# Optimization experiments

Measured on AMD Instinct MI355X. Metric: run time of the kernel, lower is better.

Reference implementation:

```python
import jax, jax.numpy as jnp
import numpy as np
import math

B, N, D, H = 256, 2048, 128, 8
HD = D // H  # 16
TANH_CLIP = 10.0
TEMP = 1.0


def setup_inputs() -> dict:
    key = jax.random.key(0)
    ks = jax.random.split(key, 10)
    context_node_projected = jax.random.normal(ks[0], (B, 1, D), dtype=jnp.float32)
    node_embeddings = jax.random.normal(ks[1], (B, N, D), dtype=jnp.float32)
    glimpse_K = jax.random.normal(ks[2], (H, B, 1, N, HD), dtype=jnp.float32)
    glimpse_V = jax.random.normal(ks[3], (H, B, 1, N, HD), dtype=jnp.float32)
    logit_K = jax.random.normal(ks[4], (B, 1, N, D), dtype=jnp.float32)
    W_ctx = jax.random.normal(ks[5], (2 * D, D), dtype=jnp.float32) * 0.05
    W_out = jax.random.normal(ks[6], (D, D), dtype=jnp.float32) * 0.05
    first_a = jax.random.randint(ks[7], (B, 1), 0, N, dtype=jnp.int32)
    current_node = jax.random.randint(ks[8], (B, 1), 0, N, dtype=jnp.int32)
    mask = jax.random.uniform(ks[9], (B, 1, N)) < 0.3
    mask = mask.at[:, :, 0].set(False)  # guarantee at least one feasible node
    return {
        "context_node_projected": context_node_projected,
        "node_embeddings": node_embeddings,
        "glimpse_K": glimpse_K,
        "glimpse_V": glimpse_V,
        "logit_K": logit_K,
        "W_ctx": W_ctx,
        "W_out": W_out,
        "first_a": first_a,
        "current_node": current_node,
        "mask": mask,
    }


def reference(context_node_projected, node_embeddings, glimpse_K, glimpse_V,
              logit_K, W_ctx, W_out, first_a, current_node, mask):
    # --- step context: gather first and current node embeddings (i > 0 branch) ---
    idx = jnp.concatenate([first_a, current_node], axis=1)          # [B, 2]
    ctx = jnp.take_along_axis(node_embeddings, idx[:, :, None], axis=1)  # [B, 2, D]
    ctx = ctx.reshape(ctx.shape[0], 1, 2 * ctx.shape[-1])           # [B, 1, 2D]
    query = context_node_projected + ctx @ W_ctx                    # [B, 1, D]

    b, steps, d = query.shape
    # glimpse_Q: [H, B, steps, 1, HD]
    glimpse_Q = query.reshape(b, steps, H, 1, HD).transpose(2, 0, 1, 3, 4)
    # compatibility: [H, B, steps, 1, N]
    compat = jnp.matmul(glimpse_Q, jnp.swapaxes(glimpse_K, -2, -1)) / math.sqrt(HD)
    # inner mask: masked positions -> -inf before softmax
    compat = jnp.where(mask[None, :, :, None, :], -jnp.inf, compat)
    attn = jax.nn.softmax(compat, axis=-1)                          # [H, B, steps, 1, N]
    heads = jnp.matmul(attn, glimpse_V)                             # [H, B, steps, 1, HD]
    # concat heads -> [B, steps, 1, D], then project_out
    heads = heads.transpose(1, 2, 3, 0, 4).reshape(b, steps, 1, H * HD)
    glimpse = heads @ W_out                                         # final_Q: [B, steps, 1, D]
    # logit attention against logit_K: [B, steps, N]
    logits = jnp.matmul(glimpse, jnp.swapaxes(logit_K, -2, -1)).squeeze(-2) / math.sqrt(d)
    logits = jnp.tanh(logits) * TANH_CLIP
    logits = jnp.where(mask, -jnp.inf, logits)
    log_p = jax.nn.log_softmax(logits / TEMP, axis=-1)              # [B, steps, N]
    return log_p
```

## Files before the change

kernel.cpp:

```cpp
#include <hip/hip_runtime.h>
#include <math.h>

#define BB 256
#define NN 2048
#define DD 128
#define HH 8
#define HDD 16

__global__ __launch_bounds__(1024) void evrp_decoder_kernel(
    const float* __restrict__ ctxproj,
    const float* __restrict__ node_emb,
    const float* __restrict__ gK,
    const float* __restrict__ gV,
    const float* __restrict__ lK,
    const float* __restrict__ Wctx,
    const float* __restrict__ Wout,
    const int*   __restrict__ first_a,
    const int*   __restrict__ cur_node,
    const unsigned char* __restrict__ mask,
    float* __restrict__ out)
{
    const int b    = blockIdx.x;
    const int tid  = threadIdx.x;
    const int lane = tid & 63;
    const int w    = tid >> 6;

    __shared__ float s_ctx[2*DD];
    __shared__ float s_q[DD];
    __shared__ float s_part[8][DD];
    __shared__ float s_heads[DD];
    __shared__ float s_g[DD];
    __shared__ float s_red[16][2+HDD];
    __shared__ unsigned char s_mask[NN];
    __shared__ float s_r[16];
    __shared__ float s_bc[2];

    s_mask[tid]        = mask[(size_t)b*NN + tid];
    s_mask[tid + 1024] = mask[(size_t)b*NN + tid + 1024];

    if (tid < DD) {
        const int i0 = first_a[b];
        const int i1 = cur_node[b];
        s_ctx[tid]      = node_emb[((size_t)b*NN + i0)*DD + tid];
        s_ctx[tid + DD] = node_emb[((size_t)b*NN + i1)*DD + tid];
    }
    __syncthreads();

    {
        const int kp = tid >> 7;
        const int d  = tid & 127;
        const int k0 = kp * 32;
        float acc = 0.f;
        #pragma unroll 8
        for (int k = 0; k < 32; ++k)
            acc = fmaf(s_ctx[k0+k], Wctx[(size_t)(k0+k)*DD + d], acc);
        s_part[kp][d] = acc;
    }
    __syncthreads();
    if (tid < DD) {
        float q = ctxproj[(size_t)b*DD + tid];
        #pragma unroll
        for (int kp = 0; kp < 8; ++kp) q += s_part[kp][tid];
        s_q[tid] = q;
    }
    __syncthreads();

    {
        const int h    = w >> 1;
        const int t128 = ((w & 1) << 6) | lane;
        float qh[HDD];
        #pragma unroll
        for (int j = 0; j < HDD; ++j) qh[j] = s_q[h*HDD + j];
        const float* __restrict__ Kh = gK + ((size_t)h*BB + b)*NN*HDD;
        const float* __restrict__ Vh = gV + ((size_t)h*BB + b)*NN*HDD;

        float m = -1e30f, s = 0.f;
        float acc[HDD];
        #pragma unroll
        for (int j = 0; j < HDD; ++j) acc[j] = 0.f;

        for (int i = 0; i < 16; ++i) {
            const int n = t128 + (i << 7);
            if (s_mask[n]) continue;
            const float4* k4 = (const float4*)(Kh + (size_t)n*HDD);
            const float4* v4 = (const float4*)(Vh + (size_t)n*HDD);
            float kk[HDD], vv[HDD];
            *(float4*)&kk[0]  = k4[0]; *(float4*)&kk[4]  = k4[1];
            *(float4*)&kk[8]  = k4[2]; *(float4*)&kk[12] = k4[3];
            *(float4*)&vv[0]  = v4[0]; *(float4*)&vv[4]  = v4[1];
            *(float4*)&vv[8]  = v4[2]; *(float4*)&vv[12] = v4[3];
            float c = 0.f;
            #pragma unroll
            for (int j = 0; j < HDD; ++j) c = fmaf(kk[j], qh[j], c);
            c *= 0.25f;
            const float mn = fmaxf(m, c);
            const float sc = expf(m - mn);
            const float p  = expf(c - mn);
            s = s * sc + p;
            #pragma unroll
            for (int j = 0; j < HDD; ++j)
                acc[j] = fmaf(acc[j], sc, p * vv[j]);
            m = mn;
        }

        #pragma unroll
        for (int off = 1; off < 64; off <<= 1) {
            const float m2 = __shfl_xor(m, off);
            const float s2 = __shfl_xor(s, off);
            const float mn = fmaxf(m, m2);
            const float e1 = expf(m - mn);
            const float e2 = expf(m2 - mn);
            s = s * e1 + s2 * e2;
            #pragma unroll
            for (int j = 0; j < HDD; ++j)
                acc[j] = acc[j] * e1 + __shfl_xor(acc[j], off) * e2;
            m = mn;
        }
        if (lane == 0) {
            s_red[w][0] = m;
            s_red[w][1] = s;
            #pragma unroll
            for (int j = 0; j < HDD; ++j) s_red[w][2+j] = acc[j];
        }
    }
    __syncthreads();

    if (((w & 1) == 0) && lane < HDD) {
        const int h = w >> 1;
        const float m1 = s_red[w][0],   s1 = s_red[w][1];
        const float m2 = s_red[w+1][0], s2 = s_red[w+1][1];
        const float mn = fmaxf(m1, m2);
        const float e1 = expf(m1 - mn), e2 = expf(m2 - mn);
        const float st = s1*e1 + s2*e2;
        const float a  = s_red[w][2+lane]*e1 + s_red[w+1][2+lane]*e2;
        s_heads[h*HDD + lane] = a / st;
    }
    __syncthreads();

    {
        const int kp = tid >> 7;
        const int d  = tid & 127;
        const int k0 = kp * 16;
        float acc = 0.f;
        #pragma unroll
        for (int k = 0; k < 16; ++k)
            acc = fmaf(s_heads[k0+k], Wout[(size_t)(k0+k)*DD + d], acc);
        s_part[kp][d] = acc;
    }
    __syncthreads();
    if (tid < DD) {
        float g = 0.f;
        #pragma unroll
        for (int kp = 0; kp < 8; ++kp) g += s_part[kp][tid];
        s_g[tid] = g;
    }
    __syncthreads();

    const float inv_sqrt_d = 0.088388347648318447f;
    float tv[2];
    #pragma unroll
    for (int i = 0; i < 2; ++i) {
        const int n = tid + (i << 10);
        if (s_mask[n]) {
            tv[i] = -1e30f;
        } else {
            const float4* r4 = (const float4*)(lK + ((size_t)b*NN + n)*DD);
            float dot = 0.f;
            #pragma unroll
            for (int jj = 0; jj < 32; ++jj) {
                const float4 f = r4[jj];
                dot = fmaf(f.x, s_g[jj*4+0], dot);
                dot = fmaf(f.y, s_g[jj*4+1], dot);
                dot = fmaf(f.z, s_g[jj*4+2], dot);
                dot = fmaf(f.w, s_g[jj*4+3], dot);
            }
            tv[i] = tanhf(dot * inv_sqrt_d) * 10.f;
        }
    }

    float lm = fmaxf(tv[0], tv[1]);
    #pragma unroll
    for (int off = 1; off < 64; off <<= 1)
        lm = fmaxf(lm, __shfl_xor(lm, off));
    if (lane == 0) s_r[w] = lm;
    __syncthreads();
    if (tid == 0) {
        float mm = -1e30f;
        #pragma unroll
        for (int i = 0; i < 16; ++i) mm = fmaxf(mm, s_r[i]);
        s_bc[0] = mm;
    }
    __syncthreads();
    const float mx = s_bc[0];

    float ls = expf(tv[0] - mx) + expf(tv[1] - mx);
    #pragma unroll
    for (int off = 1; off < 64; off <<= 1)
        ls += __shfl_xor(ls, off);
    __syncthreads();
    if (lane == 0) s_r[w] = ls;
    __syncthreads();
    if (tid == 0) {
        float ss = 0.f;
        #pragma unroll
        for (int i = 0; i < 16; ++i) ss += s_r[i];
        s_bc[1] = mx + logf(ss);
    }
    __syncthreads();
    const float lse = s_bc[1];

    out[(size_t)b*NN + tid]        = s_mask[tid]        ? -1e30f : tv[0] - lse;
    out[(size_t)b*NN + tid + 1024] = s_mask[tid + 1024] ? -1e30f : tv[1] - lse;
}

extern "C" void kernel_launch(void* const* d_in, const int* in_sizes, int n_in,
                              void* d_out, int out_size, void* d_ws, size_t ws_size,
                              hipStream_t stream) {
    const float* ctxproj  = (const float*)d_in[0];
    const float* node_emb = (const float*)d_in[1];
    const float* gK       = (const float*)d_in[2];
    const float* gV       = (const float*)d_in[3];
    const float* lK       = (const float*)d_in[4];
    const float* Wctx     = (const float*)d_in[5];
    const float* Wout     = (const float*)d_in[6];
    const int*   first_a  = (const int*)d_in[7];
    const int*   cur_node = (const int*)d_in[8];
    const unsigned char* mask = (const unsigned char*)d_in[9];
    float* out = (float*)d_out;

    hipLaunchKernelGGL(evrp_decoder_kernel, dim3(BB), dim3(1024), 0, stream,
                       ctxproj, node_emb, gK, gV, lK, Wctx, Wout,
                       first_a, cur_node, mask, out);
}
```

Baseline: 153.4 us.

## Split fused decoder into four kernels with per-head and per-segment blocks

The single 1024-thread-per-batch kernel becomes four launches: query projection, attention with one block per (batch, head), logits over 8 segments per batch with partial max/sum, and a final log-softmax normalization pass. This spreads the bandwidth-bound K/V and logit_K streaming over eight times more blocks, replacing 256 big blocks that underfill the GPU. Attention also switches from online softmax to a two-pass max-then-exp scheme. The cost is extra launches, workspace round trips, an extra read/write of the output, and the Wout projection repeated in each of the 8 segment blocks.

Result: slower. 189.1 us (+23.2%).

```diff
diff --git a/kernel.cpp b/kernel.cpp
--- a/kernel.cpp
+++ b/kernel.cpp
@@ -7,210 +7,218 @@
 #define HH 8
 #define HDD 16
 
-__global__ __launch_bounds__(1024) void evrp_decoder_kernel(
-    const float* __restrict__ ctxproj,
-    const float* __restrict__ node_emb,
-    const float* __restrict__ gK,
-    const float* __restrict__ gV,
-    const float* __restrict__ lK,
-    const float* __restrict__ Wctx,
-    const float* __restrict__ Wout,
-    const int*   __restrict__ first_a,
-    const int*   __restrict__ cur_node,
-    const unsigned char* __restrict__ mask,
-    float* __restrict__ out)
-{
-    const int b    = blockIdx.x;
+#define WSQ_OFF 0
+#define WSH_OFF 32768
+#define WSP_OFF 65536
+
+__global__ __launch_bounds__(128) void k_query(
+    const float* __restrict__ ctxproj, const float* __restrict__ node_emb,
+    const float* __restrict__ Wctx, const int* __restrict__ first_a,
+    const int* __restrict__ cur_node, float* __restrict__ wsq)
+{
+    const int b = blockIdx.x, d = threadIdx.x;
+    __shared__ float s_ctx[2*DD];
+    const int i0 = first_a[b], i1 = cur_node[b];
+    s_ctx[d]      = node_emb[((size_t)b*NN + i0)*DD + d];
+    s_ctx[d + DD] = node_emb[((size_t)b*NN + i1)*DD + d];
+    __syncthreads();
+    float q = ctxproj[(size_t)b*DD + d];
+    #pragma unroll 8
+    for (int k = 0; k < 2*DD; ++k)
+        q = fmaf(s_ctx[k], Wctx[(size_t)k*DD + d], q);
+    wsq[(size_t)b*DD + d] = q;
+}
+
+__global__ __launch_bounds__(256, 6) void k_attn(
+    const float* __restrict__ gK, const float* __restrict__ gV,
+    const unsigned char* __restrict__ mask, const float* __restrict__ wsq,
+    float* __restrict__ wsh)
+{
+    const int bid  = blockIdx.x;
+    const int b    = bid >> 3;
+    const int h    = bid & 7;
     const int tid  = threadIdx.x;
     const int lane = tid & 63;
     const int w    = tid >> 6;
 
-    __shared__ float s_ctx[2*DD];
-    __shared__ float s_q[DD];
-    __shared__ float s_part[8][DD];
-    __shared__ float s_heads[DD];
+    __shared__ unsigned char s_mask[NN];
+    __shared__ float s_q[HDD];
+    __shared__ float s_m[4];
+    __shared__ float s_red[4][1 + HDD];
+
+    ((uint2*)s_mask)[tid] = ((const uint2*)(mask + (size_t)b*NN))[tid];
+    if (tid < HDD) s_q[tid] = wsq[(size_t)b*DD + h*HDD + tid];
+    __syncthreads();
+
+    float qh[HDD];
+    #pragma unroll
+    for (int j = 0; j < HDD; ++j) qh[j] = s_q[j];
+
+    const float* __restrict__ Kh = gK + ((size_t)(h*BB + b))*NN*HDD;
+    const float* __restrict__ Vh = gV + ((size_t)(h*BB + b))*NN*HDD;
+
+    float c[8];
+    #pragma unroll
+    for (int i = 0; i < 8; ++i) {
+        const int n = tid + (i << 8);
+        if (s_mask[n]) { c[i] = -1e30f; continue; }
+        const float4* k4 = (const float4*)(Kh + (size_t)n*HDD);
+        const float4 a0 = k4[0], a1 = k4[1], a2 = k4[2], a3 = k4[3];
+        float dot = 0.f;
+        dot = fmaf(a0.x, qh[0],  dot); dot = fmaf(a0.y, qh[1],  dot);
+        dot = fmaf(a0.z, qh[2],  dot); dot = fmaf(a0.w, qh[3],  dot);
+        dot = fmaf(a1.x, qh[4],  dot); dot = fmaf(a1.y, qh[5],  dot);
+        dot = fmaf(a1.z, qh[6],  dot); dot = fmaf(a1.w, qh[7],  dot);
+        dot = fmaf(a2.x, qh[8],  dot); dot = fmaf(a2.y, qh[9],  dot);
+        dot = fmaf(a2.z, qh[10], dot); dot = fmaf(a2.w, qh[11], dot);
+        dot = fmaf(a3.x, qh[12], dot); dot = fmaf(a3.y, qh[13], dot);
+        dot = fmaf(a3.z, qh[14], dot); dot = fmaf(a3.w, qh[15], dot);
+        c[i] = dot * 0.25f;
+    }
+
+    float m = c[0];
+    #pragma unroll
+    for (int i = 1; i < 8; ++i) m = fmaxf(m, c[i]);
+    #pragma unroll
+    for (int off = 1; off < 64; off <<= 1) m = fmaxf(m, __shfl_xor(m, off));
+    if (lane == 0) s_m[w] = m;
+    __syncthreads();
+    m = fmaxf(fmaxf(s_m[0], s_m[1]), fmaxf(s_m[2], s_m[3]));
+
+    float s = 0.f;
+    float acc[HDD];
+    #pragma unroll
+    for (int j = 0; j < HDD; ++j) acc[j] = 0.f;
+
+    #pragma unroll
+    for (int i = 0; i < 8; ++i) {
+        const int n = tid + (i << 8);
+        if (s_mask[n]) continue;
+        const float p = expf(c[i] - m);
+        s += p;
+        const float4* v4 = (const float4*)(Vh + (size_t)n*HDD);
+        const float4 b0 = v4[0], b1 = v4[1], b2 = v4[2], b3 = v4[3];
+        acc[0]  = fmaf(p, b0.x, acc[0]);  acc[1]  = fmaf(p, b0.y, acc[1]);
+        acc[2]  = fmaf(p, b0.z, acc[2]);  acc[3]  = fmaf(p, b0.w, acc[3]);
+        acc[4]  = fmaf(p, b1.x, acc[4]);  acc[5]  = fmaf(p, b1.y, acc[5]);
+        acc[6]  = fmaf(p, b1.z, acc[6]);  acc[7]  = fmaf(p, b1.w, acc[7]);
+        acc[8]  = fmaf(p, b2.x, acc[8]);  acc[9]  = fmaf(p, b2.y, acc[9]);
+        acc[10] = fmaf(p, b2.z, acc[10]); acc[11] = fmaf(p, b2.w, acc[11]);
+        acc[12] = fmaf(p, b3.x, acc[12]); acc[13] = fmaf(p, b3.y, acc[13]);
+        acc[14] = fmaf(p, b3.z, acc[14]); acc[15] = fmaf(p, b3.w, acc[15]);
+    }
+
+    #pragma unroll
+    for (int off = 1; off < 64; off <<= 1) {
+        s += __shfl_xor(s, off);
+        #pragma unroll
+        for (int j = 0; j < HDD; ++j) acc[j] += __shfl_xor(acc[j], off);
+    }
+    if (lane == 0) {
+        s_red[w][0] = s;
+        #pragma unroll
+        for (int j = 0; j < HDD; ++j) s_red[w][1 + j] = acc[j];
+    }
+    __syncthreads();
+    if (w == 0 && lane < HDD) {
+        const float st = s_red[0][0] + s_red[1][0] + s_red[2][0] + s_red[3][0];
+        const float a  = s_red[0][1+lane] + s_red[1][1+lane]
+                       + s_red[2][1+lane] + s_red[3][1+lane];
+        wsh[(size_t)b*DD + h*HDD + lane] = a / st;
+    }
+}
+
+__global__ __launch_bounds__(256, 6) void k_logits(
+    const float* __restrict__ lK, const float* __restrict__ Wout,
+    const unsigned char* __restrict__ mask, const float* __restrict__ wsh,
+    float* __restrict__ out_tv, float* __restrict__ wsp)
+{
+    const int bid  = blockIdx.x;
+    const int b    = bid >> 3;
+    const int seg  = bid & 7;
+    const int tid  = threadIdx.x;
+    const int lane = tid & 63;
+    const int w    = tid >> 6;
+
+    __shared__ float s_h[DD];
+    __shared__ float s_part[2][DD];
     __shared__ float s_g[DD];
-    __shared__ float s_red[16][2+HDD];
-    __shared__ unsigned char s_mask[NN];
-    __shared__ float s_r[16];
-    __shared__ float s_bc[2];
-
-    s_mask[tid]        = mask[(size_t)b*NN + tid];
-    s_mask[tid + 1024] = mask[(size_t)b*NN + tid + 1024];
-
-    if (tid < DD) {
-        const int i0 = first_a[b];
-        const int i1 = cur_node[b];
-        s_ctx[tid]      = node_emb[((size_t)b*NN + i0)*DD + tid];
-        s_ctx[tid + DD] = node_emb[((size_t)b*NN + i1)*DD + tid];
-    }
-    __syncthreads();
-
+    __shared__ float s_rm[4];
+    __shared__ float s_rs[4];
+
+    if (tid < DD) s_h[tid] = wsh[(size_t)b*DD + tid];
+    __syncthreads();
     {
-        const int kp = tid >> 7;
-        const int d  = tid & 127;
-        const int k0 = kp * 32;
-        float acc = 0.f;
+        const int d = tid & 127, half = tid >> 7, k0 = half * 64;
+        float a = 0.f;
         #pragma unroll 8
-        for (int k = 0; k < 32; ++k)
-            acc = fmaf(s_ctx[k0+k], Wctx[(size_t)(k0+k)*DD + d], acc);
-        s_part[kp][d] = acc;
-    }
-    __syncthreads();
-    if (tid < DD) {
-        float q = ctxproj[(size_t)b*DD + tid];
+        for (int k = 0; k < 64; ++k)
+            a = fmaf(s_h[k0 + k], Wout[(size_t)(k0 + k)*DD + d], a);
+        s_part[half][d] = a;
+    }
+    __syncthreads();
+    if (tid < DD) s_g[tid] = s_part[0][tid] + s_part[1][tid];
+    __syncthreads();
+
+    const int n = (seg << 8) + tid;
+    const size_t idx = (size_t)b*NN + n;
+    const unsigned char mk = mask[idx];
+    float tv;
+    if (mk) {
+        tv = -1e30f;
+    } else {
+        const float4* r4 = (const float4*)(lK + idx*DD);
+        float dot = 0.f;
         #pragma unroll
-        for (int kp = 0; kp < 8; ++kp) q += s_part[kp][tid];
-        s_q[tid] = q;
-    }
-    __syncthreads();
-
-    {
-        const int h    = w >> 1;
-        const int t128 = ((w & 1) << 6) | lane;
-        float qh[HDD];
-        #pragma unroll
-        for (int j = 0; j < HDD; ++j) qh[j] = s_q[h*HDD + j];
-        const float* __restrict__ Kh = gK + ((size_t)h*BB + b)*NN*HDD;
-        const float* __restrict__ Vh = gV + ((size_t)h*BB + b)*NN*HDD;
-
-        float m = -1e30f, s = 0.f;
-        float acc[HDD];
-        #pragma unroll
-        for (int j = 0; j < HDD; ++j) acc[j] = 0.f;
-
-        for (int i = 0; i < 16; ++i) {
-            const int n = t128 + (i << 7);
-            if (s_mask[n]) continue;
-            const float4* k4 = (const float4*)(Kh + (size_t)n*HDD);
-            const float4* v4 = (const float4*)(Vh + (size_t)n*HDD);
-            float kk[HDD], vv[HDD];
-            *(float4*)&kk[0]  = k4[0]; *(float4*)&kk[4]  = k4[1];
-            *(float4*)&kk[8]  = k4[2]; *(float4*)&kk[12] = k4[3];
-            *(float4*)&vv[0]  = v4[0]; *(float4*)&vv[4]  = v4[1];
-            *(float4*)&vv[8]  = v4[2]; *(float4*)&vv[12] = v4[3];
-            float c = 0.f;
-            #pragma unroll
-            for (int j = 0; j < HDD; ++j) c = fmaf(kk[j], qh[j], c);
-            c *= 0.25f;
-            const float mn = fmaxf(m, c);
-            const float sc = expf(m - mn);
-            const float p  = expf(c - mn);
-            s = s * sc + p;
-            #pragma unroll
-            for (int j = 0; j < HDD; ++j)
-                acc[j] = fmaf(acc[j], sc, p * vv[j]);
-            m = mn;
+        for (int jj = 0; jj < 32; ++jj) {
+            const float4 f = r4[jj];
+            dot = fmaf(f.x, s_g[jj*4+0], dot);
+            dot = fmaf(f.y, s_g[jj*4+1], dot);
+            dot = fmaf(f.z, s_g[jj*4+2], dot);
+            dot = fmaf(f.w, s_g[jj*4+3], dot);
         }
-
-        #pragma unroll
-        for (int off = 1; off < 64; off <<= 1) {
-            const float m2 = __shfl_xor(m, off);
-            const float s2 = __shfl_xor(s, off);
-            const float mn = fmaxf(m, m2);
-            const float e1 = expf(m - mn);
-            const float e2 = expf(m2 - mn);
-            s = s * e1 + s2 * e2;
-            #pragma unroll
-            for (int j = 0; j < HDD; ++j)
-                acc[j] = acc[j] * e1 + __shfl_xor(acc[j], off) * e2;
-            m = mn;
-        }
-        if (lane == 0) {
-            s_red[w][0] = m;
-            s_red[w][1] = s;
-            #pragma unroll
-            for (int j = 0; j < HDD; ++j) s_red[w][2+j] = acc[j];
-        }
-    }
-    __syncthreads();
-
-    if (((w & 1) == 0) && lane < HDD) {
-        const int h = w >> 1;
-        const float m1 = s_red[w][0],   s1 = s_red[w][1];
-        const float m2 = s_red[w+1][0], s2 = s_red[w+1][1];
-        const float mn = fmaxf(m1, m2);
-        const float e1 = expf(m1 - mn), e2 = expf(m2 - mn);
-        const float st = s1*e1 + s2*e2;
-        const float a  = s_red[w][2+lane]*e1 + s_red[w+1][2+lane]*e2;
-        s_heads[h*HDD + lane] = a / st;
-    }
-    __syncthreads();
-
-    {
-        const int kp = tid >> 7;
-        const int d  = tid & 127;
-        const int k0 = kp * 16;
-        float acc = 0.f;
-        #pragma unroll
-        for (int k = 0; k < 16; ++k)
-            acc = fmaf(s_heads[k0+k], Wout[(size_t)(k0+k)*DD + d], acc);
-        s_part[kp][d] = acc;
-    }
-    __syncthreads();
-    if (tid < DD) {
-        float g = 0.f;
-        #pragma unroll
-        for (int kp = 0; kp < 8; ++kp) g += s_part[kp][tid];
-        s_g[tid] = g;
-    }
-    __syncthreads();
-
-    const float inv_sqrt_d = 0.088388347648318447f;
-    float tv[2];
-    #pragma unroll
-    for (int i = 0; i < 2; ++i) {
-        const int n = tid + (i << 10);
-        if (s_mask[n]) {
-            tv[i] = -1e30f;
-        } else {
-            const float4* r4 = (const float4*)(lK + ((size_t)b*NN + n)*DD);
-            float dot = 0.f;
-            #pragma unroll
-            for (int jj = 0; jj < 32; ++jj) {
-                const float4 f = r4[jj];
-                dot = fmaf(f.x, s_g[jj*4+0], dot);
-                dot = fmaf(f.y, s_g[jj*4+1], dot);
-                dot = fmaf(f.z, s_g[jj*4+2], dot);
-                dot = fmaf(f.w, s_g[jj*4+3], dot);
-            }
-            tv[i] = tanhf(dot * inv_sqrt_d) * 10.f;
-        }
-    }
-
-    float lm = fmaxf(tv[0], tv[1]);
-    #pragma unroll
-    for (int off = 1; off < 64; off <<= 1)
-        lm = fmaxf(lm, __shfl_xor(lm, off));
-    if (lane == 0) s_r[w] = lm;
-    __syncthreads();
-    if (tid == 0) {
-        float mm = -1e30f;
-        #pragma unroll
-        for (int i = 0; i < 16; ++i) mm = fmaxf(mm, s_r[i]);
-        s_bc[0] = mm;
-    }
-    __syncthreads();
-    const float mx = s_bc[0];
-
-    float ls = expf(tv[0] - mx) + expf(tv[1] - mx);
-    #pragma unroll
-    for (int off = 1; off < 64; off <<= 1)
-        ls += __shfl_xor(ls, off);
-    __syncthreads();
-    if (lane == 0) s_r[w] = ls;
-    __syncthreads();
-    if (tid == 0) {
-        float ss = 0.f;
-        #pragma unroll
-        for (int i = 0; i < 16; ++i) ss += s_r[i];
-        s_bc[1] = mx + logf(ss);
-    }
-    __syncthreads();
-    const float lse = s_bc[1];
-
-    out[(size_t)b*NN + tid]        = s_mask[tid]        ? -1e30f : tv[0] - lse;
-    out[(size_t)b*NN + tid + 1024] = s_mask[tid + 1024] ? -1e30f : tv[1] - lse;
+        tv = tanhf(dot * 0.088388347648318447f) * 10.f;
+    }
+    out_tv[idx] = tv;
+
+    float m = tv;
+    #pragma unroll
+    for (int off = 1; off < 64; off <<= 1) m = fmaxf(m, __shfl_xor(m, off));
+    if (lane == 0) s_rm[w] = m;
+    __syncthreads();
+    const float bm = fmaxf(fmaxf(s_rm[0], s_rm[1]), fmaxf(s_rm[2], s_rm[3]));
+    float e = expf(tv - bm);
+    #pragma unroll
+    for (int off = 1; off < 64; off <<= 1) e += __shfl_xor(e, off);
+    if (lane == 0) s_rs[w] = e;
+    __syncthreads();
+    if (tid == 0)
+        { wsp[(size_t)bid*2] = bm;
+          wsp[(size_t)bid*2 + 1] = s_rs[0] + s_rs[1] + s_rs[2] + s_rs[3]; }
+}
+
+__global__ __launch_bounds__(256) void k_final(
+    const unsigned char* __restrict__ mask, const float* __restrict__ wsp,
+    float* __restrict__ out)
+{
+    const int bid = blockIdx.x;
+    const int b   = bid >> 3;
+    const int seg = bid & 7;
+    const int tid = threadIdx.x;
+    __shared__ float s_p[16];
+    if (tid < 16) s_p[tid] = wsp[(size_t)b*16 + tid];
+    __syncthreads();
+    float mstar = -1e30f;
+    #pragma unroll
+    for (int i = 0; i < 8; ++i) mstar = fmaxf(mstar, s_p[2*i]);
+    float ss = 0.f;
+    #pragma unroll
+    for (int i = 0; i < 8; ++i) ss += s_p[2*i+1] * expf(s_p[2*i] - mstar);
+    const float lse = mstar + logf(ss);
+
+    const size_t idx = (size_t)b*NN + (seg << 8) + tid;
+    const float tv = out[idx];
+    out[idx] = mask[idx] ? -1e30f : tv - lse;
 }
 
 extern "C" void kernel_launch(void* const* d_in, const int* in_sizes, int n_in,
@@ -227,8 +235,18 @@
     const int*   cur_node = (const int*)d_in[8];
     const unsigned char* mask = (const unsigned char*)d_in[9];
     float* out = (float*)d_out;
-
-    hipLaunchKernelGGL(evrp_decoder_kernel, dim3(BB), dim3(1024), 0, stream,
-                       ctxproj, node_emb, gK, gV, lK, Wctx, Wout,
-                       first_a, cur_node, mask, out);
-}
+    float* ws  = (float*)d_ws;
+
+    float* wsq = ws + WSQ_OFF;
+    float* wsh = ws + WSH_OFF;
+    float* wsp = ws + WSP_OFF;
+
+    hipLaunchKernelGGL(k_query,  dim3(BB),     dim3(128), 0, stream,
+                       ctxproj, node_emb, Wctx, first_a, cur_node, wsq);
+    hipLaunchKernelGGL(k_attn,   dim3(BB*HH),  dim3(256), 0, stream,
+                       gK, gV, mask, wsq, wsh);
+    hipLaunchKernelGGL(k_logits, dim3(BB*8),   dim3(256), 0, stream,
+                       lK, Wout, mask, wsh, out, wsp);
+    hipLaunchKernelGGL(k_final,  dim3(BB*8),   dim3(256), 0, stream,
+                       mask, wsp, out);
+}
```
